# Optimization experiments

Hardware: AMD Instinct MI355X
Metric: run time of the kernel (lower is better)

The kernel has to match this reference:

```python
import jax, jax.numpy as jnp
import numpy as np

DIM = 2048
NUM_HEADS = 16
NUM_KV_HEADS = 4
HEAD_DIM = DIM // NUM_HEADS          # 128
GROUP = NUM_HEADS // NUM_KV_HEADS    # 4
ROPE_DIMS = 32                       # partial RoPE: rope_dims < head_dim
ROPE_BASE = 10000.0
QK_GAIN_INIT = 5.0
LOGIT_SOFTCAP = 30.0
BATCH = 2
SEQLEN = 2048


def setup_inputs() -> dict:
    key = jax.random.key(0)
    ks = jax.random.split(key, 5)
    x = jax.random.normal(ks[0], (BATCH, SEQLEN, DIM), dtype=jnp.float32)
    s = 0.02
    Wq = jax.random.normal(ks[1], (DIM, DIM), dtype=jnp.float32) * s
    Wk = jax.random.normal(ks[2], (NUM_KV_HEADS * HEAD_DIM, DIM), dtype=jnp.float32) * s
    Wv = jax.random.normal(ks[3], (NUM_KV_HEADS * HEAD_DIM, DIM), dtype=jnp.float32) * s
    Wproj = jax.random.normal(ks[4], (DIM, DIM), dtype=jnp.float32) * s
    q_gain = jnp.full((NUM_HEADS,), QK_GAIN_INIT, dtype=jnp.float32)
    return {"x": x, "Wq": Wq, "Wk": Wk, "Wv": Wv, "Wproj": Wproj, "q_gain": q_gain}


def _rms_norm(t):
    # torch F.rms_norm with no weight: x / sqrt(mean(x^2) + eps)
    eps = jnp.finfo(t.dtype).eps
    return t * jax.lax.rsqrt(jnp.mean(t * t, axis=-1, keepdims=True) + eps)


def _rope_tables(seqlen, dtype):
    inv_freq = 1.0 / (ROPE_BASE ** (jnp.arange(0, ROPE_DIMS, 2, dtype=jnp.float32) / ROPE_DIMS))
    t = jnp.arange(seqlen, dtype=jnp.float32)
    freqs = jnp.outer(t, inv_freq)  # [S, ROPE_DIMS/2]
    return jnp.cos(freqs).astype(dtype), jnp.sin(freqs).astype(dtype)


def _apply_rotary(x, cos, sin):
    # x: [B, S, H, D]; cos/sin: [S, rd/2]; partial rope on first rd dims
    rd = cos.shape[-1] * 2
    c = cos[None, :, None, :]
    s = sin[None, :, None, :]
    x_rope, x_pass = x[..., :rd], x[..., rd:]
    half = rd // 2
    x1, x2 = x_rope[..., :half], x_rope[..., half:]
    x_rot = jnp.concatenate((x1 * c + x2 * s, -x1 * s + x2 * c), axis=-1)
    return jnp.concatenate((x_rot, x_pass), axis=-1)


def reference(x, Wq, Wk, Wv, Wproj, q_gain):
    B, S, D = x.shape
    q = (x @ Wq.T).reshape(B, S, NUM_HEADS, HEAD_DIM)
    k = (x @ Wk.T).reshape(B, S, NUM_KV_HEADS, HEAD_DIM)
    v = (x @ Wv.T).reshape(B, S, NUM_KV_HEADS, HEAD_DIM)

    q = _rms_norm(q)
    k = _rms_norm(k)

    cos, sin = _rope_tables(S, q.dtype)
    q = _apply_rotary(q, cos, sin)
    k = _apply_rotary(k, cos, sin)

    q = q * q_gain.astype(q.dtype)[None, None, :, None]

    # GQA causal attention with logit softcap; SDPA default scale 1/sqrt(head_dim)
    scale = 1.0 / np.sqrt(HEAD_DIM)
    qg = q.reshape(B, S, NUM_KV_HEADS, GROUP, HEAD_DIM)
    scores = jnp.einsum('bqhgd,bkhd->bhgqk', qg, k) * scale  # [B,Hkv,G,S,S]
    scores = LOGIT_SOFTCAP * jnp.tanh(scores / LOGIT_SOFTCAP)
    causal = jnp.tril(jnp.ones((S, S), dtype=bool))
    scores = jnp.where(causal[None, None, None], scores, -jnp.inf)
    attn = jax.nn.softmax(scores, axis=-1)
    y = jnp.einsum('bhgqk,bkhd->bqhgd', attn, v)  # [B,S,Hkv,G,D]
    y = y.reshape(B, S, NUM_HEADS * HEAD_DIM)

    return y @ Wproj.T
```

## Files before the change

### kernel.cpp

```cpp
#include <hip/hip_runtime.h>
#include <type_traits>

#define BATCH 2
#define S_LEN 2048
#define DIM 2048
#define NH 16
#define NKV 4
#define HD 128

typedef _Float16 f16x8 __attribute__((ext_vector_type(8)));
typedef float f32x4 __attribute__((ext_vector_type(4)));
typedef unsigned int u32x4 __attribute__((ext_vector_type(4)));
typedef unsigned short u16x4 __attribute__((ext_vector_type(4)));
typedef unsigned short u16x8 __attribute__((ext_vector_type(8)));

__device__ __forceinline__ unsigned short f2h_bits(float f) {
  _Float16 h = (_Float16)f;
  return __builtin_bit_cast(unsigned short, h);
}
__device__ __forceinline__ float h2f(unsigned short u) {
  return (float)__builtin_bit_cast(_Float16, u);
}
__device__ __forceinline__ f16x8 ld8(const unsigned short* p) {
  u32x4 v = *reinterpret_cast<const u32x4*>(p);
  return __builtin_bit_cast(f16x8, v);
}
__device__ __forceinline__ void gload_lds16(const unsigned short* g, unsigned short* l) {
  __builtin_amdgcn_global_load_lds(
      (const __attribute__((address_space(1))) unsigned int*)g,
      (__attribute__((address_space(3))) unsigned int*)l, 16, 0, 0);
}

#define VMWAIT(n) asm volatile("s_waitcnt vmcnt(" #n ")" ::: "memory")

__global__ __launch_bounds__(256) void cvt_all(const float* __restrict__ x,
                                               const float* __restrict__ Wq,
                                               const float* __restrict__ Wk,
                                               const float* __restrict__ Wv,
                                               const float* __restrict__ Wp,
                                               unsigned short* __restrict__ xb,
                                               unsigned short* __restrict__ wqkv,
                                               unsigned short* __restrict__ wpj) {
  int i = blockIdx.x * 256 + threadIdx.x;
  const float* src;
  unsigned short* dst;
  if (i < 2097152) {
    src = x + (long)i * 4; dst = xb + (long)i * 4;
  } else if (i < 3145728) {
    int k = i - 2097152; src = Wq + (long)k * 4; dst = wqkv + (long)k * 4;
  } else if (i < 3407872) {
    int k = i - 3145728; src = Wk + (long)k * 4; dst = wqkv + 4194304 + (long)k * 4;
  } else if (i < 3670016) {
    int k = i - 3407872; src = Wv + (long)k * 4; dst = wqkv + 5242880 + (long)k * 4;
  } else {
    int k = i - 3670016; src = Wp + (long)k * 4; dst = wpj + (long)k * 4;
  }
  f32x4 v = *reinterpret_cast<const f32x4*>(src);
  u16x4 o;
  o.x = f2h_bits(v.x); o.y = f2h_bits(v.y); o.z = f2h_bits(v.z); o.w = f2h_bits(v.w);
  *reinterpret_cast<u16x4*>(dst) = o;
}

__global__ __launch_bounds__(256) void rope_tables(float* __restrict__ c, float* __restrict__ s) {
  int idx = blockIdx.x * 256 + threadIdx.x;
  if (idx >= S_LEN * 16) return;
  int i = idx & 15, t = idx >> 4;
  float inv = exp2f(-(float)i * (13.287712379549449f / 16.0f));
  float f = (float)t * inv;
  c[idx] = cosf(f);
  s[idx] = sinf(f);
}

template <int NREP, typename OUT>
__global__ __launch_bounds__(512, 2) void gemm_pl(const unsigned short* __restrict__ A,
                                                  const unsigned short* __restrict__ B,
                                                  OUT* __restrict__ C, int K, int ldc) {
  constexpr int BN = 64 * NREP;
  constexpr int BSH = BN * 32;
  constexpr int TS = 8192 + BSH;
  __shared__ unsigned short lds[4][TS];
  const int tid = threadIdx.x, lane = tid & 63;
  const int wm = tid >> 8, wn = (tid >> 6) & 3;
  const int rlo = lane & 15, hi = lane >> 4;
  const int m0 = blockIdx.x * 256, n0 = blockIdx.y * BN;
  const int NT = K >> 5;
  const int brow = wn * (16 * NREP);

  auto aRow = [&](int sig) { return (sig & 63) + ((sig >> 6) & 1) * 128 + (sig >> 7) * 64; };

  const int sigA0 = tid >> 2, sigA1 = 128 + (tid >> 2);
  const unsigned short* pA0 =
      A + (long)(m0 + aRow(sigA0)) * K + (((tid & 3) ^ ((sigA0 >> 1) & 3)) * 8);
  const unsigned short* pA1 =
      A + (long)(m0 + aRow(sigA1)) * K + (((tid & 3) ^ ((sigA1 >> 1) & 3)) * 8);
  const int rB0 = tid >> 2;
  const unsigned short* pB0 = B + (long)(n0 + rB0) * K + (((tid & 3) ^ ((rB0 >> 1) & 3)) * 8);
  const int idx1 = 512 + (tid & 255);
  const int rB1 = idx1 >> 2;
  const unsigned short* pB1 = B + (long)(n0 + rB1) * K + (((idx1 & 3) ^ ((rB1 >> 1) & 3)) * 8);

  auto stage = [&](int slot) {
    gload_lds16(pA0, &lds[slot][tid * 8]);
    gload_lds16(pA1, &lds[slot][4096 + tid * 8]);
    gload_lds16(pB0, &lds[slot][8192 + tid * 8]);
    if constexpr (NREP == 3) gload_lds16(pB1, &lds[slot][8192 + idx1 * 8]);
    pA0 += 32; pA1 += 32; pB0 += 32;
    if constexpr (NREP == 3) pB1 += 32;
  };

  f32x4 acc[8][NREP] = {};

  auto rdA = [&](const unsigned short* As, int mh, f16x8* af) {
#pragma unroll
    for (int i = 0; i < 4; ++i) {
      int ms = mh * 4 + i;
      int sig = (ms & 3) * 16 + rlo + wm * 64 + (ms >> 2) * 128;
      af[i] = ld8(&As[sig * 32 + ((hi ^ ((sig >> 1) & 3)) * 8)]);
    }
  };
  auto rdB = [&](const unsigned short* Bs, f16x8* bf) {
#pragma unroll
    for (int j = 0; j < NREP; ++j) {
      int r = brow + j * 16 + rlo;
      bf[j] = ld8(&Bs[r * 32 + ((hi ^ ((r >> 1) & 3)) * 8)]);
    }
  };
  auto mm = [&](const f16x8* af, const f16x8* bf, int mh) {
    __builtin_amdgcn_s_setprio(1);
#pragma unroll
    for (int i = 0; i < 4; ++i)
#pragma unroll
      for (int j = 0; j < NREP; ++j)
        acc[mh * 4 + i][j] =
            __builtin_amdgcn_mfma_f32_16x16x32_f16(af[i], bf[j], acc[mh * 4 + i][j], 0, 0, 0);
    __builtin_amdgcn_s_setprio(0);
  };

  stage(0);
  stage(1);
  for (int t = 0; t < NT; ++t) {
    const int slot = t & 3;
    if (t == NT - 1) {
      VMWAIT(0);
    } else {
      if constexpr (NREP == 3) VMWAIT(4); else VMWAIT(3);
    }
    __builtin_amdgcn_s_barrier();
    asm volatile("" ::: "memory");
    if (t + 2 < NT) stage((t + 2) & 3);
    const unsigned short* As = &lds[slot][0];
    const unsigned short* Bs = &lds[slot][8192];
    f16x8 bf[NREP], af0[4], af1[4];
    rdB(Bs, bf);
    rdA(As, 0, af0);
    rdA(As, 1, af1);
    mm(af0, bf, 0);
    mm(af1, bf, 1);
  }

#pragma unroll
  for (int ms = 0; ms < 8; ++ms)
#pragma unroll
    for (int j = 0; j < NREP; ++j) {
      int row = m0 + wm * 128 + ms * 16 + hi * 4;
      int col = n0 + brow + j * 16 + rlo;
#pragma unroll
      for (int r = 0; r < 4; ++r) {
        float v = acc[ms][j][r];
        if constexpr (std::is_same<OUT, float>::value)
          C[(long)(row + r) * ldc + col] = v;
        else
          C[(long)(row + r) * ldc + col] = f2h_bits(v);
      }
    }
}

__global__ __launch_bounds__(256) void qknorm_rope(const unsigned short* __restrict__ qkv,
                                                   const float* __restrict__ ctab,
                                                   const float* __restrict__ stab,
                                                   const float* __restrict__ qgain,
                                                   unsigned short* __restrict__ Qb,
                                                   unsigned short* __restrict__ Kb) {
  const int lane = threadIdx.x & 63;
  const int row = blockIdx.x * 4 + (threadIdx.x >> 6);
  const int NQROWS = BATCH * S_LEN * NH;
  const unsigned short* src;
  unsigned short* dst;
  int m, hh;
  bool isQ;
  if (row < NQROWS) {
    m = row >> 4; hh = row & 15;
    src = qkv + (long)m * 3072 + hh * HD;
    int b = m >> 11, s = m & (S_LEN - 1);
    dst = Qb + (((long)(b * NH + hh)) * S_LEN + s) * HD;
    isQ = true;
  } else {
    int rk = row - NQROWS;
    m = rk >> 2; hh = rk & 3;
    src = qkv + (long)m * 3072 + 2048 + hh * HD;
    int b = m >> 11, s = m & (S_LEN - 1);
    dst = Kb + (((long)(b * NKV + hh)) * S_LEN + s) * HD;
    isQ = false;
  }
  const int s = m & (S_LEN - 1);
  float x0 = h2f(src[lane]);
  float x1 = h2f(src[lane + 64]);
  float ss = x0 * x0 + x1 * x1;
  ss += __shfl_xor(ss, 1); ss += __shfl_xor(ss, 2); ss += __shfl_xor(ss, 4);
  ss += __shfl_xor(ss, 8); ss += __shfl_xor(ss, 16); ss += __shfl_xor(ss, 32);
  float rn = rsqrtf(ss * (1.0f / 128.0f) + 1.1920929e-07f);
  float n0 = x0 * rn, n1 = x1 * rn;
  float partner = __shfl_xor(n0, 16);
  if (lane < 32) {
    int i = lane & 15;
    float c = ctab[s * 16 + i], sn = stab[s * 16 + i];
    n0 = (lane < 16) ? (n0 * c + partner * sn) : (n0 * c - partner * sn);
  }
  if (isQ) { float g = qgain[hh]; n0 *= g; n1 *= g; }
  dst[lane] = f2h_bits(n0);
  dst[lane + 64] = f2h_bits(n1);
}

__global__ __launch_bounds__(256) void vtrans(const unsigned short* __restrict__ qkv,
                                              unsigned short* __restrict__ Vt) {
  int idx = blockIdx.x * 256 + threadIdx.x;
  int d = idx & 127;
  int sc = (idx >> 7) & 255;
  int kvh = (idx >> 15) & 3;
  int b = idx >> 17;
  u16x8 v;
#pragma unroll
  for (int j = 0; j < 8; ++j)
    v[j] = qkv[((long)(b * S_LEN + sc * 8 + j)) * 3072 + 2560 + kvh * HD + d];
  *reinterpret_cast<u16x8*>(Vt + (((long)(b * NKV + kvh)) * HD + d) * S_LEN + sc * 8) = v;
}

#define ATT_C3 ((float)(0.08838834764831845 * (2.0 / 30.0) * 1.4426950408889634))
#define ATT_C4 ((float)(30.0 * 1.4426950408889634))
#define ATT_C5 ((float)(60.0 * 1.4426950408889634))
#define ATT_THR ((float)(8.0 * 1.4426950408889634))

__global__ __launch_bounds__(256, 4) void attn(const unsigned short* __restrict__ Qb,
                                               const unsigned short* __restrict__ Kb,
                                               const unsigned short* __restrict__ Vt,
                                               unsigned short* __restrict__ Yb) {
  __shared__ unsigned short sm[2][8192];
  const int tid = threadIdx.x, wid = tid >> 6, lane = tid & 63;
  const int gx = blockIdx.x;
  const int qq = gx >> 8;
  const int a = (gx >> 5) & 7;
  const int h = gx & 15, b = (gx >> 4) & 1;
  int qb;
  if (qq == 0) qb = 31 - a;
  else if (qq == 1) qb = 16 + a;
  else if (qq == 2) qb = 15 - a;
  else qb = a;

  const int kvh = h >> 2;
  const int rlo = lane & 15, hi = lane >> 4;
  const int q0 = qb * 64 + wid * 16;
  const unsigned short* Kp = Kb + ((long)(b * NKV + kvh)) * S_LEN * HD;
  const unsigned short* Vp = Vt + ((long)(b * NKV + kvh)) * HD * S_LEN;
  const unsigned short* Qp = Qb + (((long)(b * NH + h)) * S_LEN + q0) * HD;
  f16x8 bq[4];
#pragma unroll
  for (int dk = 0; dk < 4; ++dk) bq[dk] = ld8(Qp + rlo * HD + dk * 32 + hi * 8);

  const int kx = rlo & 7;
  const int vx = hi ^ ((rlo >> 1) & 3);
  const unsigned short* aK[4];
#pragma unroll
  for (int dk = 0; dk < 4; ++dk) aK[dk] = &sm[0][rlo * 128 + ((dk * 4 + hi) ^ kx) * 8];
  const unsigned short* aV = &sm[0][4096 + rlo * 32 + vx * 8];

  const int i0 = tid, i1 = tid + 256;
  const int rho0 = i0 >> 4, rho1 = i1 >> 4;
  auto kvperm = [](int r) { return 8 * ((r >> 2) & 3) + (r & 3) + 4 * (r >> 4); };
  const unsigned short* sK0 = Kp + (long)kvperm(rho0) * HD + ((i0 & 15) ^ (rho0 & 7)) * 8;
  const unsigned short* sK1 = Kp + (long)kvperm(rho1) * HD + ((i1 & 15) ^ (rho1 & 7)) * 8;
  const int vd0 = i0 >> 2, vd1 = i1 >> 2;
  const unsigned short* sV0 = Vp + (long)vd0 * S_LEN + ((i0 & 3) ^ ((vd0 >> 1) & 3)) * 8;
  const unsigned short* sV1 = Vp + (long)vd1 * S_LEN + ((i1 & 3) ^ ((vd1 >> 1) & 3)) * 8;
  unsigned short* dK0 = &sm[0][rho0 * 128 + (i0 & 15) * 8];
  unsigned short* dK1 = &sm[0][rho1 * 128 + (i1 & 15) * 8];
  unsigned short* dV0 = &sm[0][4096 + vd0 * 32 + (i0 & 3) * 8];
  unsigned short* dV1 = &sm[0][4096 + vd1 * 32 + (i1 & 3) * 8];

  f32x4 acc[8] = {};
  float m2c = ATT_C4 + 128.0f;
  float l_run = 0.0f;
  const int nt = 2 * qb + 2;
  const int twlast = 2 * qb + (wid >> 1);

#define STAGE(SLOT)                                                       \
  {                                                                       \
    gload_lds16(sK0, dK0 + (SLOT)*8192);                                  \
    gload_lds16(sK1, dK1 + (SLOT)*8192);                                  \
    gload_lds16(sV0, dV0 + (SLOT)*8192);                                  \
    gload_lds16(sV1, dV1 + (SLOT)*8192);                                  \
    sK0 += 4096; sK1 += 4096; sV0 += 32; sV1 += 32;                       \
  }

#define COMPUTE(T, SLOT)                                                              \
  {                                                                                   \
    f16x8 ka0[4], ka1[4];                                                             \
    _Pragma("unroll")                                                                 \
    for (int dk = 0; dk < 4; ++dk) {                                                  \
      ka0[dk] = ld8(aK[dk] + (SLOT)*8192);                                            \
      ka1[dk] = ld8(aK[dk] + (SLOT)*8192 + 2048);                                     \
    }                                                                                 \
    f32x4 s0 = {0.f, 0.f, 0.f, 0.f}, s1 = s0;                                         \
    __builtin_amdgcn_s_setprio(1);                                                    \
    _Pragma("unroll")                                                                 \
    for (int dk = 0; dk < 4; ++dk) {                                                  \
      s0 = __builtin_amdgcn_mfma_f32_16x16x32_f16(ka0[dk], bq[dk], s0, 0, 0, 0);      \
      s1 = __builtin_amdgcn_mfma_f32_16x16x32_f16(ka1[dk], bq[dk], s1, 0, 0, 0);      \
    }                                                                                 \
    __builtin_amdgcn_s_setprio(0);                                                    \
    float ea[8];                                                                      \
    _Pragma("unroll")                                                                 \
    for (int jj = 0; jj < 8; ++jj) {                                                  \
      float sc = (jj < 4) ? s0[jj] : s1[jj - 4];                                      \
      float u = __builtin_amdgcn_exp2f(sc * ATT_C3);                                  \
      float rr = __builtin_amdgcn_rcpf(u + 1.0f);                                     \
      ea[jj] = fmaf(-ATT_C5, rr, m2c);                                                \
    }                                                                                 \
    if ((T) == twlast) {                                                              \
      int qrel = q0 + rlo - 32 * (T);                                                 \
      _Pragma("unroll")                                                               \
      for (int jj = 0; jj < 8; ++jj)                                                  \
        ea[jj] = (8 * hi + jj > qrel) ? -1e30f : ea[jj];                              \
    }                                                                                 \
    float pm = ea[0];                                                                 \
    _Pragma("unroll")                                                                 \
    for (int jj = 1; jj < 8; ++jj) pm = fmaxf(pm, ea[jj]);                            \
    if (!__all(pm <= ATT_THR)) {                                                      \
      float red = fmaxf(pm, __shfl_xor(pm, 16));                                      \
      red = fmaxf(red, __shfl_xor(red, 32));                                          \
      red = fmaxf(red, 0.0f);                                                         \
      m2c -= red;                                                                     \
      float ff = __builtin_amdgcn_exp2f(-red);                                        \
      l_run *= ff;                                                                    \
      _Pragma("unroll")                                                               \
      for (int dt = 0; dt < 8; ++dt) acc[dt] *= ff;                                   \
      _Pragma("unroll")                                                               \
      for (int jj = 0; jj < 8; ++jj) ea[jj] -= red;                                   \
    }                                                                                 \
    float pv[8];                                                                      \
    _Pragma("unroll")                                                                 \
    for (int jj = 0; jj < 8; ++jj) pv[jj] = __builtin_amdgcn_exp2f(ea[jj]);           \
    l_run += ((pv[0] + pv[1]) + (pv[2] + pv[3])) + ((pv[4] + pv[5]) + (pv[6] + pv[7]));\
    u32x4 pk;                                                                         \
    pk.x = __builtin_bit_cast(unsigned int, __builtin_amdgcn_cvt_pkrtz(pv[0], pv[1]));\
    pk.y = __builtin_bit_cast(unsigned int, __builtin_amdgcn_cvt_pkrtz(pv[2], pv[3]));\
    pk.z = __builtin_bit_cast(unsigned int, __builtin_amdgcn_cvt_pkrtz(pv[4], pv[5]));\
    pk.w = __builtin_bit_cast(unsigned int, __builtin_amdgcn_cvt_pkrtz(pv[6], pv[7]));\
    f16x8 bp = __builtin_bit_cast(f16x8, pk);                                         \
    __builtin_amdgcn_s_setprio(1);                                                    \
    _Pragma("unroll")                                                                 \
    for (int g = 0; g < 2; ++g) {                                                     \
      f16x8 av[4];                                                                    \
      _Pragma("unroll")                                                               \
      for (int i = 0; i < 4; ++i) av[i] = ld8(aV + (SLOT)*8192 + (g * 4 + i) * 512);  \
      _Pragma("unroll")                                                               \
      for (int i = 0; i < 4; ++i)                                                     \
        acc[g * 4 + i] =                                                              \
            __builtin_amdgcn_mfma_f32_16x16x32_f16(av[i], bp, acc[g * 4 + i], 0, 0, 0);\
    }                                                                                 \
    __builtin_amdgcn_s_setprio(0);                                                    \
  }

  STAGE(0);
  for (int t = 0; t < nt; t += 2) {
    VMWAIT(0);
    __builtin_amdgcn_s_barrier();
    asm volatile("" ::: "memory");
    STAGE(1);
    if (t <= twlast) COMPUTE(t, 0);
    VMWAIT(0);
    __builtin_amdgcn_s_barrier();
    asm volatile("" ::: "memory");
    if (t + 2 < nt) STAGE(0);
    if (t + 1 <= twlast) COMPUTE(t + 1, 1);
  }
#undef STAGE
#undef COMPUTE

  float l = l_run + __shfl_xor(l_run, 16);
  l += __shfl_xor(l, 32);
  float inv = 1.0f / l;
  unsigned short* yp = Yb + ((long)(b * S_LEN + q0 + rlo)) * DIM + h * HD + 4 * hi;
#pragma unroll
  for (int dt = 0; dt < 8; ++dt) {
    u16x4 o;
#pragma unroll
    for (int r = 0; r < 4; ++r) o[r] = f2h_bits(acc[dt][r] * inv);
    *reinterpret_cast<u16x4*>(yp + dt * 16) = o;
  }
}

extern "C" void kernel_launch(void* const* d_in, const int* in_sizes, int n_in,
                              void* d_out, int out_size, void* d_ws, size_t ws_size,
                              hipStream_t stream) {
  const float* x = (const float*)d_in[0];
  const float* Wq = (const float*)d_in[1];
  const float* Wk = (const float*)d_in[2];
  const float* Wv = (const float*)d_in[3];
  const float* Wp = (const float*)d_in[4];
  const float* qg = (const float*)d_in[5];
  float* out = (float*)d_out;

  char* ws = (char*)d_ws;
  size_t off = 0;
  auto alloc = [&](size_t bytes) {
    char* p = ws + off;
    off += (bytes + 255) & ~(size_t)255;
    return p;
  };
  unsigned short* xb   = (unsigned short*)alloc(8388608ull * 2);
  unsigned short* wqkv = (unsigned short*)alloc(6291456ull * 2);
  unsigned short* wpj  = (unsigned short*)alloc(4194304ull * 2);
  unsigned short* qkv  = (unsigned short*)alloc(4096ull * 3072 * 2);
  unsigned short* Qbuf = (unsigned short*)alloc(8388608ull * 2);
  unsigned short* Kb   = (unsigned short*)alloc(2097152ull * 2);
  unsigned short* Vt   = (unsigned short*)alloc(2097152ull * 2);
  unsigned short* Yb   = (unsigned short*)alloc(8388608ull * 2);
  float* ctab = (float*)alloc(32768ull * 4);
  float* stab = (float*)alloc(32768ull * 4);

  cvt_all<<<18432, 256, 0, stream>>>(x, Wq, Wk, Wv, Wp, xb, wqkv, wpj);
  rope_tables<<<128, 256, 0, stream>>>(ctab, stab);

  gemm_pl<3, unsigned short><<<dim3(16, 16), 512, 0, stream>>>(xb, wqkv, qkv, 2048, 3072);

  qknorm_rope<<<(BATCH * S_LEN * (NH + NKV)) / 4, 256, 0, stream>>>(qkv, ctab, stab, qg, Qbuf, Kb);
  vtrans<<<(BATCH * NKV * HD * (S_LEN / 8)) / 256, 256, 0, stream>>>(qkv, Vt);

  attn<<<1024, 256, 0, stream>>>(Qbuf, Kb, Vt, Yb);

  gemm_pl<2, float><<<dim3(16, 16), 512, 0, stream>>>(Yb, wpj, out, 2048, 2048);
}
```

Baseline: 195.8 us.

## Fuse QK RMSNorm, RoPE, gain and V transpose into QKV GEMM epilogue

Replaces the generic QKV GEMM plus separate qknorm_rope and vtrans kernels with a dedicated GEMM. Each 128-column tile maps to exactly one head, so the epilogue does the row RMS norm (cross-wave reduction through LDS), partial RoPE, q_gain scaling and direct writes to the head-major Q/K layout and the transposed V layout. This removes the qkv intermediate buffer round trip and two kernel launches. In exchange the tile shrinks to 128x128 with 256 threads, which may lower GEMM efficiency, and the V stores are scattered 8-byte writes.

```diff
diff --git a/kernel.cpp b/kernel.cpp
--- a/kernel.cpp
+++ b/kernel.cpp
@@ -71,6 +71,130 @@
   s[idx] = sinf(f);
 }
 
+__global__ __launch_bounds__(256, 2) void gemm_qkv(const unsigned short* __restrict__ A,
+                                                   const unsigned short* __restrict__ B,
+                                                   const float* __restrict__ ctab,
+                                                   const float* __restrict__ stab,
+                                                   const float* __restrict__ qgain,
+                                                   unsigned short* __restrict__ Qb,
+                                                   unsigned short* __restrict__ Kb,
+                                                   unsigned short* __restrict__ Vt) {
+  __shared__ unsigned short lds[4][8192];
+  const int tid = threadIdx.x, lane = tid & 63;
+  const int wm = (tid >> 7) & 1, wn = (tid >> 6) & 1;
+  const int rlo = lane & 15, hi = lane >> 4;
+  const int m0 = blockIdx.x * 128;
+  const int by = blockIdx.y;
+  const int n0 = by * 128;
+  const int K = 2048, NT = 64;
+
+  const int i0 = tid, i1 = tid + 256;
+  const int ar0 = i0 >> 2, ar1 = i1 >> 2;
+  const unsigned short* pA0 = A + (long)(m0 + ar0) * K + (((i0 & 3) ^ ((ar0 >> 1) & 3)) * 8);
+  const unsigned short* pA1 = A + (long)(m0 + ar1) * K + (((i1 & 3) ^ ((ar1 >> 1) & 3)) * 8);
+  const unsigned short* pB0 = B + (long)(n0 + ar0) * K + (((i0 & 3) ^ ((ar0 >> 1) & 3)) * 8);
+  const unsigned short* pB1 = B + (long)(n0 + ar1) * K + (((i1 & 3) ^ ((ar1 >> 1) & 3)) * 8);
+
+  auto stage = [&](int slot) {
+    gload_lds16(pA0, &lds[slot][i0 * 8]);
+    gload_lds16(pA1, &lds[slot][i1 * 8]);
+    gload_lds16(pB0, &lds[slot][4096 + i0 * 8]);
+    gload_lds16(pB1, &lds[slot][4096 + i1 * 8]);
+    pA0 += 32; pA1 += 32; pB0 += 32; pB1 += 32;
+  };
+
+  f32x4 acc[4][4] = {};
+
+  stage(0);
+  stage(1);
+  for (int t = 0; t < NT; ++t) {
+    const int slot = t & 3;
+    if (t == NT - 1) VMWAIT(0); else VMWAIT(4);
+    __builtin_amdgcn_s_barrier();
+    asm volatile("" ::: "memory");
+    if (t + 2 < NT) stage((t + 2) & 3);
+    const unsigned short* As = &lds[slot][0];
+    const unsigned short* Bs = &lds[slot][4096];
+    f16x8 af[4], bf[4];
+#pragma unroll
+    for (int j = 0; j < 4; ++j) {
+      int r = wn * 64 + j * 16 + rlo;
+      bf[j] = ld8(&Bs[r * 32 + ((hi ^ ((r >> 1) & 3)) * 8)]);
+    }
+#pragma unroll
+    for (int i2 = 0; i2 < 4; ++i2) {
+      int r = wm * 64 + i2 * 16 + rlo;
+      af[i2] = ld8(&As[r * 32 + ((hi ^ ((r >> 1) & 3)) * 8)]);
+    }
+    __builtin_amdgcn_s_setprio(1);
+#pragma unroll
+    for (int i2 = 0; i2 < 4; ++i2)
+#pragma unroll
+      for (int j = 0; j < 4; ++j)
+        acc[i2][j] = __builtin_amdgcn_mfma_f32_16x16x32_f16(af[i2], bf[j], acc[i2][j], 0, 0, 0);
+    __builtin_amdgcn_s_setprio(0);
+  }
+
+  __syncthreads();
+  if (by < 20) {
+    float* fs = (float*)&lds[0][0];
+#pragma unroll
+    for (int ms = 0; ms < 4; ++ms)
+#pragma unroll
+      for (int rr = 0; rr < 4; ++rr) {
+        float p = acc[ms][0][rr] * acc[ms][0][rr] + acc[ms][1][rr] * acc[ms][1][rr] +
+                  acc[ms][2][rr] * acc[ms][2][rr] + acc[ms][3][rr] * acc[ms][3][rr];
+        p += __shfl_xor(p, 1); p += __shfl_xor(p, 2);
+        p += __shfl_xor(p, 4); p += __shfl_xor(p, 8);
+        if (rlo == ms * 4 + rr) fs[wn * 128 + wm * 64 + ms * 16 + hi * 4 + rr] = p;
+      }
+    __syncthreads();
+    const bool isQ = by < 16;
+    const int hh = isQ ? by : (by - 16);
+    const float g = isQ ? qgain[hh] : 1.0f;
+#pragma unroll
+    for (int ms = 0; ms < 4; ++ms)
+#pragma unroll
+      for (int rr = 0; rr < 4; ++rr) {
+        int rowb = wm * 64 + ms * 16 + hi * 4 + rr;
+        int m = m0 + rowb;
+        int b = m >> 11, s = m & (S_LEN - 1);
+        float rs = fs[rowb] + fs[128 + rowb];
+        float rn = rsqrtf(rs * (1.0f / 128.0f) + 1.1920929e-07f);
+        float v0 = acc[ms][0][rr] * rn, v1 = acc[ms][1][rr] * rn;
+        float v2 = acc[ms][2][rr] * rn, v3 = acc[ms][3][rr] * rn;
+        if (wn == 0) {
+          float c = ctab[s * 16 + rlo], sn = stab[s * 16 + rlo];
+          float a0 = v0, a1 = v1;
+          v0 = a0 * c + a1 * sn;
+          v1 = -a0 * sn + a1 * c;
+        }
+        unsigned short* dst = (isQ ? Qb + (((long)(b * NH + hh)) * S_LEN + s) * HD
+                                   : Kb + (((long)(b * NKV + hh)) * S_LEN + s) * HD) +
+                              wn * 64 + rlo;
+        dst[0]  = f2h_bits(v0 * g);
+        dst[16] = f2h_bits(v1 * g);
+        dst[32] = f2h_bits(v2 * g);
+        dst[48] = f2h_bits(v3 * g);
+      }
+  } else {
+    const int kvh = by - 20;
+#pragma unroll
+    for (int ms = 0; ms < 4; ++ms) {
+      int m = m0 + wm * 64 + ms * 16 + hi * 4;
+      int b = m >> 11, s = m & (S_LEN - 1);
+#pragma unroll
+      for (int j = 0; j < 4; ++j) {
+        int d = wn * 64 + j * 16 + rlo;
+        u16x4 o;
+#pragma unroll
+        for (int rr = 0; rr < 4; ++rr) o[rr] = f2h_bits(acc[ms][j][rr]);
+        *reinterpret_cast<u16x4*>(Vt + (((long)(b * NKV + kvh)) * HD + d) * S_LEN + s) = o;
+      }
+    }
+  }
+}
+
 template <int NREP, typename OUT>
 __global__ __launch_bounds__(512, 2) void gemm_pl(const unsigned short* __restrict__ A,
                                                   const unsigned short* __restrict__ B,
@@ -173,66 +297,6 @@
           C[(long)(row + r) * ldc + col] = f2h_bits(v);
       }
     }
-}
-
-__global__ __launch_bounds__(256) void qknorm_rope(const unsigned short* __restrict__ qkv,
-                                                   const float* __restrict__ ctab,
-                                                   const float* __restrict__ stab,
-                                                   const float* __restrict__ qgain,
-                                                   unsigned short* __restrict__ Qb,
-                                                   unsigned short* __restrict__ Kb) {
-  const int lane = threadIdx.x & 63;
-  const int row = blockIdx.x * 4 + (threadIdx.x >> 6);
-  const int NQROWS = BATCH * S_LEN * NH;
-  const unsigned short* src;
-  unsigned short* dst;
-  int m, hh;
-  bool isQ;
-  if (row < NQROWS) {
-    m = row >> 4; hh = row & 15;
-    src = qkv + (long)m * 3072 + hh * HD;
-    int b = m >> 11, s = m & (S_LEN - 1);
-    dst = Qb + (((long)(b * NH + hh)) * S_LEN + s) * HD;
-    isQ = true;
-  } else {
-    int rk = row - NQROWS;
-    m = rk >> 2; hh = rk & 3;
-    src = qkv + (long)m * 3072 + 2048 + hh * HD;
-    int b = m >> 11, s = m & (S_LEN - 1);
-    dst = Kb + (((long)(b * NKV + hh)) * S_LEN + s) * HD;
-    isQ = false;
-  }
-  const int s = m & (S_LEN - 1);
-  float x0 = h2f(src[lane]);
-  float x1 = h2f(src[lane + 64]);
-  float ss = x0 * x0 + x1 * x1;
-  ss += __shfl_xor(ss, 1); ss += __shfl_xor(ss, 2); ss += __shfl_xor(ss, 4);
-  ss += __shfl_xor(ss, 8); ss += __shfl_xor(ss, 16); ss += __shfl_xor(ss, 32);
-  float rn = rsqrtf(ss * (1.0f / 128.0f) + 1.1920929e-07f);
-  float n0 = x0 * rn, n1 = x1 * rn;
-  float partner = __shfl_xor(n0, 16);
-  if (lane < 32) {
-    int i = lane & 15;
-    float c = ctab[s * 16 + i], sn = stab[s * 16 + i];
-    n0 = (lane < 16) ? (n0 * c + partner * sn) : (n0 * c - partner * sn);
-  }
-  if (isQ) { float g = qgain[hh]; n0 *= g; n1 *= g; }
-  dst[lane] = f2h_bits(n0);
-  dst[lane + 64] = f2h_bits(n1);
-}
-
-__global__ __launch_bounds__(256) void vtrans(const unsigned short* __restrict__ qkv,
-                                              unsigned short* __restrict__ Vt) {
-  int idx = blockIdx.x * 256 + threadIdx.x;
-  int d = idx & 127;
-  int sc = (idx >> 7) & 255;
-  int kvh = (idx >> 15) & 3;
-  int b = idx >> 17;
-  u16x8 v;
-#pragma unroll
-  for (int j = 0; j < 8; ++j)
-    v[j] = qkv[((long)(b * S_LEN + sc * 8 + j)) * 3072 + 2560 + kvh * HD + d];
-  *reinterpret_cast<u16x8*>(Vt + (((long)(b * NKV + kvh)) * HD + d) * S_LEN + sc * 8) = v;
 }
 
 #define ATT_C3 ((float)(0.08838834764831845 * (2.0 / 30.0) * 1.4426950408889634))
@@ -420,7 +484,6 @@
   unsigned short* xb   = (unsigned short*)alloc(8388608ull * 2);
   unsigned short* wqkv = (unsigned short*)alloc(6291456ull * 2);
   unsigned short* wpj  = (unsigned short*)alloc(4194304ull * 2);
-  unsigned short* qkv  = (unsigned short*)alloc(4096ull * 3072 * 2);
   unsigned short* Qbuf = (unsigned short*)alloc(8388608ull * 2);
   unsigned short* Kb   = (unsigned short*)alloc(2097152ull * 2);
   unsigned short* Vt   = (unsigned short*)alloc(2097152ull * 2);
@@ -431,10 +494,7 @@
   cvt_all<<<18432, 256, 0, stream>>>(x, Wq, Wk, Wv, Wp, xb, wqkv, wpj);
   rope_tables<<<128, 256, 0, stream>>>(ctab, stab);
 
-  gemm_pl<3, unsigned short><<<dim3(16, 16), 512, 0, stream>>>(xb, wqkv, qkv, 2048, 3072);
-
-  qknorm_rope<<<(BATCH * S_LEN * (NH + NKV)) / 4, 256, 0, stream>>>(qkv, ctab, stab, qg, Qbuf, Kb);
-  vtrans<<<(BATCH * NKV * HD * (S_LEN / 8)) / 256, 256, 0, stream>>>(qkv, Vt);
+  gemm_qkv<<<dim3(32, 24), 256, 0, stream>>>(xb, wqkv, ctab, stab, qg, Qbuf, Kb, Vt);
 
   attn<<<1024, 256, 0, stream>>>(Qbuf, Kb, Vt, Yb);
 
```

New measurement: 192.0 us. About the same (-2.0%).
